# Kernel tuning notes

Measured on AMD Instinct MI355X. Metric: run time of the kernel, lower is better.

Reference implementation:

```python
import jax, jax.numpy as jnp
import numpy as np


def setup_inputs() -> dict:
    key = jax.random.key(0)
    ks = jax.random.split(key, 6)
    H = 1024
    NB = 5
    B = H  # required by the module's gate broadcasting (gate shape [B] * candidate [B,H])
    T = 128
    return {
        "features": jax.random.normal(ks[0], (B, T, H), dtype=jnp.float32),
        "states": jax.random.normal(ks[1], (NB * H,), dtype=jnp.float32),
        "Uw": jax.random.normal(ks[2], (H, H), dtype=jnp.float32) * 0.02,
        "Vw": jax.random.normal(ks[3], (H, H), dtype=jnp.float32) * 0.02,
        "Ww": jax.random.normal(ks[4], (H, H), dtype=jnp.float32) * 0.02,
        "keys": jax.random.normal(ks[5], (NB, H), dtype=jnp.float32) * 0.02,
        "prelu_a": jnp.ones((H,), dtype=jnp.float32),
    }


def reference(features, states, Uw, Vw, Ww, keys, prelu_a):
    # features: [B, T, H]; take CLS token (input_all_tokens=True)
    enc = features[:, 0, :]                      # [B, H]
    NB, H = keys.shape
    h = states.reshape(NB, H)                    # chunked states, [NB, H]

    # gate_i = sigmoid(enc @ h_i + enc @ key_i), vectorized over blocks -> [B, NB]
    gate = jax.nn.sigmoid(enc @ (h + keys).T)

    # candidate_i = PReLU(U(h_i) + V(key_i) + W(enc)) -> [NB, B, H]
    pre = (h @ Uw.T + keys @ Vw.T)[:, None, :] + (enc @ Ww.T)[None, :, :]
    cand = jnp.where(pre >= 0, pre, prelu_a * pre)

    # torch broadcasting of gate [B] against [B, H] aligns trailing dims (B == H),
    # so gate indexes the FEATURE axis: new[i, b, j] = h[i, j] + gate[j, i] * cand[i, b, j]
    new = h[:, None, :] + gate.T[:, None, :] * cand  # [NB, B, H]

    # in-place zero replacement aliases hidden_i in the original, so zeros -> 0.1 -> 1 after normalize
    new = jnp.where(new == 0, jnp.asarray(0.1, new.dtype), new)
    new = new / jnp.abs(new)

    # torch.cat(new_states) along dim 0 -> [NB*B, H]
    return new.reshape(NB * new.shape[1], H)
```

## Files before the change

### kernel.cpp

```cpp
#include <hip/hip_runtime.h>

#define H 1024
#define NB 5
#define TSTRIDE 131072

#define BM 64
#define BN 64
#define BK 32
#define LDA 68

__device__ __forceinline__ float sign_val(float h, float g, float pre, float a) {
    float cand = (pre >= 0.0f) ? pre : a * pre;
    float v = h + g * cand;
    if (v == 0.0f) v = 0.1f;
    return (v > 0.0f) ? 1.0f : -1.0f;
}

__global__ __launch_bounds__(256) void prep_kernel(
    const float* __restrict__ features,
    const float* __restrict__ states,
    const float* __restrict__ Uw,
    const float* __restrict__ Vw,
    const float* __restrict__ keys,
    float* __restrict__ gateT,
    float* __restrict__ baseT)
{
    const int j = blockIdx.x;
    const int tid = threadIdx.x;
    float accg[NB] = {0.f, 0.f, 0.f, 0.f, 0.f};
    float accb[NB] = {0.f, 0.f, 0.f, 0.f, 0.f};
    const float* encRow = features + (size_t)j * TSTRIDE;
    const float* uRow = Uw + (size_t)j * H;
    const float* vRow = Vw + (size_t)j * H;
    for (int k = tid; k < H; k += 256) {
        const float e = encRow[k];
        const float u = uRow[k];
        const float v = vRow[k];
        #pragma unroll
        for (int n = 0; n < NB; ++n) {
            const float hk = states[n * H + k];
            const float ky = keys[n * H + k];
            accg[n] += e * (hk + ky);
            accb[n] += hk * u + ky * v;
        }
    }
    __shared__ float red[2 * NB][4];
    #pragma unroll
    for (int n = 0; n < NB; ++n) {
        float g = accg[n], b = accb[n];
        #pragma unroll
        for (int off = 32; off > 0; off >>= 1) {
            g += __shfl_down(g, (unsigned)off, 64);
            b += __shfl_down(b, (unsigned)off, 64);
        }
        if ((tid & 63) == 0) {
            red[n][tid >> 6] = g;
            red[NB + n][tid >> 6] = b;
        }
    }
    __syncthreads();
    if (tid < 2 * NB) {
        const float s = red[tid][0] + red[tid][1] + red[tid][2] + red[tid][3];
        if (tid < NB) {
            gateT[tid * H + j] = 1.0f / (1.0f + expf(-s));
        } else {
            baseT[(tid - NB) * H + j] = s;
        }
    }
}

__global__ __launch_bounds__(256) void gemm_sign_kernel(
    const float* __restrict__ features,
    const float* __restrict__ Ww,
    const float* __restrict__ states,
    const float* __restrict__ prelu_a,
    const float* __restrict__ gateT,
    const float* __restrict__ baseT,
    float* __restrict__ out)
{
    __shared__ float As[BK][LDA];
    __shared__ float Bs[BK][LDA];
    const int bb = blockIdx.y * BM;
    const int jb = blockIdx.x * BN;
    const int tid = (int)threadIdx.x;
    const int tx = tid & 15;
    const int ty = tid >> 4;

    float acc[4][4] = {};

    for (int k0 = 0; k0 < H; k0 += BK) {
        #pragma unroll
        for (int l = 0; l < 2; ++l) {
            const int f = tid + l * 256;
            const int row = f >> 3;
            const int kq = (f & 7) << 2;
            const float4 av = *(const float4*)(features + (size_t)(bb + row) * TSTRIDE + k0 + kq);
            const float4 bv = *(const float4*)(Ww + (size_t)(jb + row) * H + k0 + kq);
            As[kq + 0][row] = av.x; As[kq + 1][row] = av.y;
            As[kq + 2][row] = av.z; As[kq + 3][row] = av.w;
            Bs[kq + 0][row] = bv.x; Bs[kq + 1][row] = bv.y;
            Bs[kq + 2][row] = bv.z; Bs[kq + 3][row] = bv.w;
        }
        __syncthreads();
        #pragma unroll
        for (int kk = 0; kk < BK; ++kk) {
            const float4 a = *(const float4*)&As[kk][ty << 2];
            const float4 b = *(const float4*)&Bs[kk][tx << 2];
            acc[0][0] += a.x * b.x; acc[0][1] += a.x * b.y; acc[0][2] += a.x * b.z; acc[0][3] += a.x * b.w;
            acc[1][0] += a.y * b.x; acc[1][1] += a.y * b.y; acc[1][2] += a.y * b.z; acc[1][3] += a.y * b.w;
            acc[2][0] += a.z * b.x; acc[2][1] += a.z * b.y; acc[2][2] += a.z * b.z; acc[2][3] += a.z * b.w;
            acc[3][0] += a.w * b.x; acc[3][1] += a.w * b.y; acc[3][2] += a.w * b.z; acc[3][3] += a.w * b.w;
        }
        __syncthreads();
    }

    const int c = jb + (tx << 2);
    const float4 pa = *(const float4*)(prelu_a + c);
    #pragma unroll
    for (int n = 0; n < NB; ++n) {
        const float4 hv = *(const float4*)(states + n * H + c);
        const float4 gv = *(const float4*)(gateT + n * H + c);
        const float4 sv = *(const float4*)(baseT + n * H + c);
        #pragma unroll
        for (int i = 0; i < 4; ++i) {
            float4 o;
            o.x = sign_val(hv.x, gv.x, sv.x + acc[i][0], pa.x);
            o.y = sign_val(hv.y, gv.y, sv.y + acc[i][1], pa.y);
            o.z = sign_val(hv.z, gv.z, sv.z + acc[i][2], pa.z);
            o.w = sign_val(hv.w, gv.w, sv.w + acc[i][3], pa.w);
            const int row = bb + (ty << 2) + i;
            *(float4*)(out + ((size_t)(n * H + row) * H + c)) = o;
        }
    }
}

extern "C" void kernel_launch(void* const* d_in, const int* in_sizes, int n_in,
                              void* d_out, int out_size, void* d_ws, size_t ws_size,
                              hipStream_t stream) {
    const float* features = (const float*)d_in[0];
    const float* states   = (const float*)d_in[1];
    const float* Uw       = (const float*)d_in[2];
    const float* Vw       = (const float*)d_in[3];
    const float* Ww       = (const float*)d_in[4];
    const float* keys     = (const float*)d_in[5];
    const float* prelu_a  = (const float*)d_in[6];
    float* out = (float*)d_out;

    float* gateT = (float*)d_ws;
    float* baseT = gateT + NB * H;

    prep_kernel<<<H, 256, 0, stream>>>(features, states, Uw, Vw, keys, gateT, baseT);

    dim3 grid(H / BN, H / BM);
    gemm_sign_kernel<<<grid, 256, 0, stream>>>(features, Ww, states, prelu_a,
                                               gateT, baseT, out);
}
```

Baseline: 643.2 us.

## Double-buffer GEMM smem tiles with XOR swizzle and vectorize prep loads

The GEMM kernel now uses two shared-memory buffers and register prefetch, so global loads for the next K tile are issued before computing on the current one. It also drops the padded layout in favour of an XOR swizzle to avoid bank conflicts, and needs only one barrier per K step. The prep kernel replaces its strided loop with a single float4 load per thread, and the sign function is simplified to v >= 0. The cost is twice the shared memory and more registers held across the loop.

```diff
diff --git a/kernel.cpp b/kernel.cpp
--- a/kernel.cpp
+++ b/kernel.cpp
@@ -7,13 +7,11 @@
 #define BM 64
 #define BN 64
 #define BK 32
-#define LDA 68
 
 __device__ __forceinline__ float sign_val(float h, float g, float pre, float a) {
     float cand = (pre >= 0.0f) ? pre : a * pre;
     float v = h + g * cand;
-    if (v == 0.0f) v = 0.1f;
-    return (v > 0.0f) ? 1.0f : -1.0f;
+    return (v >= 0.0f) ? 1.0f : -1.0f;
 }
 
 __global__ __launch_bounds__(256) void prep_kernel(
@@ -26,24 +24,24 @@
     float* __restrict__ baseT)
 {
     const int j = blockIdx.x;
-    const int tid = threadIdx.x;
-    float accg[NB] = {0.f, 0.f, 0.f, 0.f, 0.f};
-    float accb[NB] = {0.f, 0.f, 0.f, 0.f, 0.f};
-    const float* encRow = features + (size_t)j * TSTRIDE;
-    const float* uRow = Uw + (size_t)j * H;
-    const float* vRow = Vw + (size_t)j * H;
-    for (int k = tid; k < H; k += 256) {
-        const float e = encRow[k];
-        const float u = uRow[k];
-        const float v = vRow[k];
-        #pragma unroll
-        for (int n = 0; n < NB; ++n) {
-            const float hk = states[n * H + k];
-            const float ky = keys[n * H + k];
-            accg[n] += e * (hk + ky);
-            accb[n] += hk * u + ky * v;
-        }
+    const int tid = (int)threadIdx.x;
+    const int k4 = tid << 2;
+
+    const float4 e = *(const float4*)(features + (size_t)j * TSTRIDE + k4);
+    const float4 u = *(const float4*)(Uw + (size_t)j * H + k4);
+    const float4 v = *(const float4*)(Vw + (size_t)j * H + k4);
+
+    float accg[NB], accb[NB];
+    #pragma unroll
+    for (int n = 0; n < NB; ++n) {
+        const float4 hk = *(const float4*)(states + n * H + k4);
+        const float4 ky = *(const float4*)(keys + n * H + k4);
+        accg[n] = e.x * (hk.x + ky.x) + e.y * (hk.y + ky.y)
+                + e.z * (hk.z + ky.z) + e.w * (hk.w + ky.w);
+        accb[n] = hk.x * u.x + hk.y * u.y + hk.z * u.z + hk.w * u.w
+                + ky.x * v.x + ky.y * v.y + ky.z * v.z + ky.w * v.w;
     }
+
     __shared__ float red[2 * NB][4];
     #pragma unroll
     for (int n = 0; n < NB; ++n) {
@@ -69,6 +67,15 @@
     }
 }
 
+__device__ __forceinline__ void stash_tile(float (*dst)[64], int row, int kq, float4 v) {
+    const int g = row >> 2, r = row & 3;
+    const int col = ((g ^ (kq >> 2)) << 2) | r;
+    dst[kq + 0][col] = v.x;
+    dst[kq + 1][col] = v.y;
+    dst[kq + 2][col] = v.z;
+    dst[kq + 3][col] = v.w;
+}
+
 __global__ __launch_bounds__(256) void gemm_sign_kernel(
     const float* __restrict__ features,
     const float* __restrict__ Ww,
@@ -78,38 +85,63 @@
     const float* __restrict__ baseT,
     float* __restrict__ out)
 {
-    __shared__ float As[BK][LDA];
-    __shared__ float Bs[BK][LDA];
+    __shared__ float As[2][BK][64];
+    __shared__ float Bs[2][BK][64];
     const int bb = blockIdx.y * BM;
     const int jb = blockIdx.x * BN;
     const int tid = (int)threadIdx.x;
     const int tx = tid & 15;
     const int ty = tid >> 4;
 
+    const int row0 = tid >> 3;
+    const int kq   = (tid & 7) << 2;
+    const float* aptr0 = features + (size_t)(bb + row0) * TSTRIDE + kq;
+    const float* aptr1 = features + (size_t)(bb + row0 + 32) * TSTRIDE + kq;
+    const float* bptr0 = Ww + (size_t)(jb + row0) * H + kq;
+    const float* bptr1 = Ww + (size_t)(jb + row0 + 32) * H + kq;
+
     float acc[4][4] = {};
 
-    for (int k0 = 0; k0 < H; k0 += BK) {
-        #pragma unroll
-        for (int l = 0; l < 2; ++l) {
-            const int f = tid + l * 256;
-            const int row = f >> 3;
-            const int kq = (f & 7) << 2;
-            const float4 av = *(const float4*)(features + (size_t)(bb + row) * TSTRIDE + k0 + kq);
-            const float4 bv = *(const float4*)(Ww + (size_t)(jb + row) * H + k0 + kq);
-            As[kq + 0][row] = av.x; As[kq + 1][row] = av.y;
-            As[kq + 2][row] = av.z; As[kq + 3][row] = av.w;
-            Bs[kq + 0][row] = bv.x; Bs[kq + 1][row] = bv.y;
-            Bs[kq + 2][row] = bv.z; Bs[kq + 3][row] = bv.w;
+    {
+        const float4 a0 = *(const float4*)(aptr0);
+        const float4 a1 = *(const float4*)(aptr1);
+        const float4 b0 = *(const float4*)(bptr0);
+        const float4 b1 = *(const float4*)(bptr1);
+        stash_tile(As[0], row0,      kq, a0);
+        stash_tile(As[0], row0 + 32, kq, a1);
+        stash_tile(Bs[0], row0,      kq, b0);
+        stash_tile(Bs[0], row0 + 32, kq, b1);
+    }
+    __syncthreads();
+
+    const int NT = H / BK;
+    for (int t = 0; t < NT; ++t) {
+        const int cur = t & 1;
+        float4 a0, a1, b0, b1;
+        const bool pf = (t + 1 < NT);
+        if (pf) {
+            const int off = (t + 1) * BK;
+            a0 = *(const float4*)(aptr0 + off);
+            a1 = *(const float4*)(aptr1 + off);
+            b0 = *(const float4*)(bptr0 + off);
+            b1 = *(const float4*)(bptr1 + off);
         }
-        __syncthreads();
         #pragma unroll
         for (int kk = 0; kk < BK; ++kk) {
-            const float4 a = *(const float4*)&As[kk][ty << 2];
-            const float4 b = *(const float4*)&Bs[kk][tx << 2];
+            const int sw = kk >> 2;
+            const float4 a = *(const float4*)&As[cur][kk][(ty ^ sw) << 2];
+            const float4 b = *(const float4*)&Bs[cur][kk][(tx ^ sw) << 2];
             acc[0][0] += a.x * b.x; acc[0][1] += a.x * b.y; acc[0][2] += a.x * b.z; acc[0][3] += a.x * b.w;
             acc[1][0] += a.y * b.x; acc[1][1] += a.y * b.y; acc[1][2] += a.y * b.z; acc[1][3] += a.y * b.w;
             acc[2][0] += a.z * b.x; acc[2][1] += a.z * b.y; acc[2][2] += a.z * b.z; acc[2][3] += a.z * b.w;
             acc[3][0] += a.w * b.x; acc[3][1] += a.w * b.y; acc[3][2] += a.w * b.z; acc[3][3] += a.w * b.w;
+        }
+        if (pf) {
+            const int nxt = cur ^ 1;
+            stash_tile(As[nxt], row0,      kq, a0);
+            stash_tile(As[nxt], row0 + 32, kq, a1);
+            stash_tile(Bs[nxt], row0,      kq, b0);
+            stash_tile(Bs[nxt], row0 + 32, kq, b1);
         }
         __syncthreads();
     }
```

New measurement: 630.6 us. About the same (-2.0%).
